# Kernel tuning notes

Hardware: AMD Instinct MI355X
Metric: run time of the kernel (lower is better)

Reference implementation:

```python
import jax, jax.numpy as jnp
import numpy as np

B, HIMG, WIMG = 256, 64, 64
U, K, HID, O, A, V = 8, 4, 128, 4, 7, 400
EMB = ((HIMG - 1) // 2 - 2) * ((WIMG - 1) // 2 - 2) * 64  # 53824
CV = EMB // U  # comm value size 6728
DK, DKC = 64, 32  # input / comm attention key sizes


def conv2d(x, w, b):
    y = jax.lax.conv_general_dilated(x, w, (1, 1), 'VALID',
                                     dimension_numbers=('NCHW', 'OIHW', 'NCHW'))
    return y + b[None, :, None, None]


def maxpool2(x):
    return jax.lax.reduce_window(x, -jnp.inf, jax.lax.max,
                                 (1, 1, 2, 2), (1, 1, 2, 2), 'VALID')


def setup_inputs() -> dict:
    key = jax.random.key(0)
    ks = jax.random.split(key, 26)
    n = lambda i, shape, sc: (jax.random.normal(ks[i], shape, jnp.float32) * sc)
    return {
        'x': jax.random.uniform(ks[0], (B, HIMG, WIMG, 3), jnp.float32),
        'hx': n(1, (B, U, HID), 0.1),
        'cx': n(2, (B, U, HID), 0.1),
        'option': jax.random.uniform(ks[3], (B, O), jnp.float32),
        'conv1_w': n(4, (16, 3, 2, 2), 0.2), 'conv1_b': jnp.zeros((16,), jnp.float32),
        'conv2_w': n(5, (32, 16, 2, 2), 0.1), 'conv2_b': jnp.zeros((32,), jnp.float32),
        'conv3_w': n(6, (64, 32, 2, 2), 0.08), 'conv3_b': jnp.zeros((64,), jnp.float32),
        'Wk': n(7, (EMB, DK), 0.01), 'bk': jnp.zeros((DK,), jnp.float32),
        'Wv': n(8, (EMB, V), 0.01), 'bv': jnp.zeros((V,), jnp.float32),
        'Wq': n(9, (O, U, HID, DK), 0.05),
        'Wi': n(10, (U, V, 4 * HID), 0.05),
        'Wh': n(11, (U, HID, 4 * HID), 0.05),
        'b_lstm': jnp.zeros((U, 4 * HID), jnp.float32),
        'Wqc': n(12, (U, HID, DKC), 0.05),
        'Wkc': n(13, (U, HID, DKC), 0.05),
        'Wvc': n(14, (U, HID, CV), 0.05),
        'Wout': n(15, (U, CV, HID), 0.01),
        'pi_w': n(16, (O, HID, A), 0.05),
        'pi_b': n(17, (O, A), 0.05),
    }


def reference(x, hx, cx, option, conv1_w, conv1_b, conv2_w, conv2_b, conv3_w,
              conv3_b, Wk, bk, Wv, bv, Wq, Wi, Wh, b_lstm, Wqc, Wkc, Wvc,
              Wout, pi_w, pi_b):
    # conv trunk: NHWC -> NCHW (as torch transposes), conv/relu/pool stack
    h = jnp.transpose(x, (0, 3, 1, 2))
    h = maxpool2(jax.nn.relu(conv2d(h, conv1_w, conv1_b)))
    h = jax.nn.relu(conv2d(h, conv2_w, conv2_b))
    h = jax.nn.relu(conv2d(h, conv3_w, conv3_b))
    emb = h.reshape(h.shape[0], -1)  # (B, EMB)

    # RIM input attention: real input + null row, per-unit option-conditioned queries
    xin = jnp.stack([emb, jnp.zeros_like(emb)], axis=1)     # (B, 2, EMB)
    k_in = xin @ Wk + bk                                     # (B, 2, DK)
    v_in = xin @ Wv + bv                                     # (B, 2, V)
    Wq_o = jnp.einsum('bo,ouhk->buhk', option, Wq)           # option-selected query weights
    q = jnp.einsum('buh,buhk->buk', hx, Wq_o)                # (B, U, DK)
    scores = jnp.einsum('buk,bnk->bun', q, k_in) / jnp.sqrt(jnp.float32(DK))
    probs = jax.nn.softmax(scores, axis=-1)                  # (B, U, 2)
    attn_in = jnp.einsum('bun,bnv->buv', probs, v_in)        # (B, U, V)

    # top-k active-unit mask (units attending most to the real input)
    real = probs[:, :, 0]
    _, idx = jax.lax.top_k(real, K)
    mask = jnp.zeros((real.shape[0], U), real.dtype)
    mask = mask.at[jnp.arange(real.shape[0])[:, None], idx].set(1.0)

    # per-unit LSTM (grouped weights)
    pre = (jnp.einsum('buv,uvg->bug', attn_in, Wi)
           + jnp.einsum('buh,uhg->bug', hx, Wh) + b_lstm)
    i_g, f_g, g_g, o_g = jnp.split(pre, 4, axis=-1)
    c_new = jax.nn.sigmoid(f_g) * cx + jax.nn.sigmoid(i_g) * jnp.tanh(g_g)
    h_new = jax.nn.sigmoid(o_g) * jnp.tanh(c_new)

    # communication attention among units; inactive queries masked out
    qc = jnp.einsum('buh,uhk->buk', h_new, Wqc)
    kc = jnp.einsum('buh,uhk->buk', h_new, Wkc)
    vc = jnp.einsum('buh,uhv->buv', h_new, Wvc)              # (B, U, CV)
    cs = jnp.einsum('buk,bnk->bun', qc, kc) / jnp.sqrt(jnp.float32(DKC))
    cp = jax.nn.softmax(cs, axis=-1) * mask[:, :, None]
    ctx = jnp.einsum('bun,bnv->buv', cp, vc)                 # (B, U, CV)
    h_comm = h_new + jnp.einsum('buv,uvh->buh', ctx, Wout)

    m = mask[:, :, None]
    hy = m * h_comm + (1.0 - m) * hx
    cy = m * c_new + (1.0 - m) * cx

    logits = jnp.einsum('buh,oha->boa', hy, pi_w) + pi_b     # (B, O, A)
    action_probs = jax.nn.softmax(logits, axis=-1)
    return action_probs, hy, cy
```

## Files before the change

### kernel.cpp

```cpp
#include <hip/hip_runtime.h>
#include <math.h>

namespace {
constexpr int NB  = 256;
constexpr int NU  = 8;
constexpr int NKT = 4;
constexpr int NH  = 128;
constexpr int NO  = 4;
constexpr int NA  = 7;
constexpr int NV  = 400;
constexpr int NE  = 53824;
constexpr int NCV = 6728;
constexpr int NDK = 64;
constexpr int NDKC= 32;

constexpr int H1 = 31, W1 = 31;
constexpr int H2 = 30, W2 = 30;
constexpr int H3 = 29, W3 = 29;
}

typedef __attribute__((ext_vector_type(8))) short bf16x8_t;
typedef __attribute__((ext_vector_type(4))) float f32x4_t;

__device__ __forceinline__ unsigned short f2bf(float f) {
    unsigned int u = __float_as_uint(f);
    u += 0x7FFFu + ((u >> 16) & 1u);
    return (unsigned short)(u >> 16);
}
__device__ __forceinline__ float bf2f(unsigned short h) {
    return __uint_as_float((unsigned int)h << 16);
}

__global__ __launch_bounds__(256)
void k_conv1(const float* __restrict__ x, const float* __restrict__ w,
             const float* __restrict__ bias, float* __restrict__ out)
{
    __shared__ float ws[16*3*2*2];
    __shared__ float bs[16];
    int tid = threadIdx.x;
    if (tid < 192) ws[tid] = w[tid];
    if (tid < 16)  bs[tid] = bias[tid];
    __syncthreads();
    long idx = (long)blockIdx.x*256 + tid;
    if (idx >= (long)NB*16*H1*W1) return;
    int pw = idx % W1; long t = idx / W1;
    int ph = t % H1; t /= H1;
    int oc = t % 16; int b = t / 16;
    float mx = 0.f;
#pragma unroll
    for (int dh = 0; dh < 2; ++dh)
#pragma unroll
    for (int dw = 0; dw < 2; ++dw) {
        int h = 2*ph + dh, ww = 2*pw + dw;
        float s = bs[oc];
#pragma unroll
        for (int kh = 0; kh < 2; ++kh)
#pragma unroll
        for (int kw = 0; kw < 2; ++kw) {
            const float* xp = x + (((long)b*64 + (h+kh))*64 + (ww+kw))*3;
#pragma unroll
            for (int ic = 0; ic < 3; ++ic)
                s += xp[ic] * ws[((oc*3+ic)*2+kh)*2+kw];
        }
        mx = fmaxf(mx, s);
    }
    out[idx] = mx;
}

template<int OC, int IC, int HIN, int WIN, int HOUT, int WOUT>
__global__ __launch_bounds__(256)
void conv2x2_gemm(const float* __restrict__ in, const float* __restrict__ w,
                  const float* __restrict__ bias, float* __restrict__ out)
{
    constexpr int K    = IC*4;
    constexpr int TY   = OC/4;
    constexpr int TX   = 256/TY;
    constexpr int NT   = TX*4;
    constexpr int SPAT = HOUT*WOUT;
    constexpr int NBLK = (SPAT + NT - 1)/NT;

    const int b  = blockIdx.x / NBLK;
    const int n0 = (blockIdx.x % NBLK) * NT;

    __shared__ __align__(16) float As[16][OC+4];
    __shared__ __align__(16) float Bs[16][NT];

    const int tid = threadIdx.x;
    const int tx = tid % TX, ty = tid / TX;
    float acc[4][4] = {};
    const float* inb = in + (long)b*IC*HIN*WIN;

    for (int kk = 0; kk < K; kk += 16) {
#pragma unroll
        for (int i = 0; i < OC*16/256; ++i) {
            int lin = tid + i*256;
            int m = lin / 16, k = lin % 16;
            As[k][m] = w[m*K + kk + k];
        }
#pragma unroll
        for (int i = 0; i < 16*NT/256; ++i) {
            int lin = tid + i*256;
            int k = lin / NT, n = lin % NT;
            int gk = kk + k;
            int ic = gk >> 2, tap = gk & 3;
            int s = n0 + n;
            float v = 0.f;
            if (s < SPAT) {
                int oh = s / WOUT, ow = s % WOUT;
                v = inb[(ic*HIN + oh + (tap>>1))*WIN + ow + (tap&1)];
            }
            Bs[k][n] = v;
        }
        __syncthreads();
#pragma unroll
        for (int k = 0; k < 16; ++k) {
            float4 a4 = *reinterpret_cast<const float4*>(&As[k][ty*4]);
            float4 b4 = *reinterpret_cast<const float4*>(&Bs[k][tx*4]);
            float av[4] = {a4.x,a4.y,a4.z,a4.w};
            float bw[4] = {b4.x,b4.y,b4.z,b4.w};
#pragma unroll
            for (int i = 0; i < 4; ++i)
#pragma unroll
            for (int j = 0; j < 4; ++j) acc[i][j] += av[i]*bw[j];
        }
        __syncthreads();
    }
#pragma unroll
    for (int i = 0; i < 4; ++i) {
        int gm = ty*4 + i;
        float bi = bias[gm];
#pragma unroll
        for (int j = 0; j < 4; ++j) {
            int s = n0 + tx*4 + j;
            if (s < SPAT)
                out[((long)b*OC + gm)*SPAT + s] = fmaxf(acc[i][j] + bi, 0.f);
        }
    }
}

__global__ __launch_bounds__(256)
void k_cvt(const float* __restrict__ in, unsigned short* __restrict__ out, long n)
{
    long i = ((long)blockIdx.x*256 + threadIdx.x) * 8;
    if (i >= n) return;
    float4 a = *(const float4*)(in + i);
    float4 b = *(const float4*)(in + i + 4);
    uint4 u;
    u.x = (unsigned)f2bf(a.x) | ((unsigned)f2bf(a.y) << 16);
    u.y = (unsigned)f2bf(a.z) | ((unsigned)f2bf(a.w) << 16);
    u.z = (unsigned)f2bf(b.x) | ((unsigned)f2bf(b.y) << 16);
    u.w = (unsigned)f2bf(b.z) | ((unsigned)f2bf(b.w) << 16);
    *(uint4*)(out + i) = u;
}

__global__ __launch_bounds__(256)
void k_f2bt(const float* __restrict__ in, unsigned short* __restrict__ out,
            int R, int Cc, long sIn)
{
    __shared__ unsigned short t[32][33];
    const int b = blockIdx.z;
    const int r0 = blockIdx.y * 32, c0 = blockIdx.x * 32;
    const float* ip = in + (long)b * sIn;
    unsigned short* op = out + (long)b * sIn;
    const int tid = threadIdx.x;
    {
        int rr = tid >> 3, c4 = (tid & 7) * 4;
        int gr = r0 + rr;
        unsigned short h0=0,h1=0,h2=0,h3=0;
        if (gr < R) {
            if (c0 + c4 + 3 < Cc) {
                float4 f = *(const float4*)(ip + (long)gr*Cc + c0 + c4);
                h0=f2bf(f.x); h1=f2bf(f.y); h2=f2bf(f.z); h3=f2bf(f.w);
            } else {
                if (c0+c4+0 < Cc) h0 = f2bf(ip[(long)gr*Cc + c0+c4+0]);
                if (c0+c4+1 < Cc) h1 = f2bf(ip[(long)gr*Cc + c0+c4+1]);
                if (c0+c4+2 < Cc) h2 = f2bf(ip[(long)gr*Cc + c0+c4+2]);
                if (c0+c4+3 < Cc) h3 = f2bf(ip[(long)gr*Cc + c0+c4+3]);
            }
        }
        t[rr][c4+0]=h0; t[rr][c4+1]=h1; t[rr][c4+2]=h2; t[rr][c4+3]=h3;
    }
    __syncthreads();
    {
        int cc = tid >> 3, r4 = (tid & 7) * 4;
        int gc = c0 + cc;
        if (gc < Cc && r0 + r4 < R) {
            if (r0 + r4 + 3 < R) {
                *(ushort4*)(op + (long)gc*R + r0 + r4) =
                    make_ushort4(t[r4+0][cc], t[r4+1][cc], t[r4+2][cc], t[r4+3][cc]);
            } else {
#pragma unroll
                for (int j = 0; j < 4; ++j)
                    if (r0 + r4 + j < R) op[(long)gc*R + r0 + r4 + j] = t[r4+j][cc];
            }
        }
    }
}

template<int ROWS, bool F32>
__device__ __forceinline__ void stage_tile(const void* __restrict__ Av, long lda,
                                           int m0, int kk, int kEnd, int Mlim,
                                           unsigned short* lds, int tid)
{
#pragma unroll
    for (int i = 0; i < ROWS/64; ++i) {
        int row = (tid >> 2) + i*64;
        int blk = tid & 3;
        long gm = m0 + row;
        long gk = kk + blk*8;
        ushort4 lo = make_ushort4(0,0,0,0), hi = make_ushort4(0,0,0,0);
        if (gm < Mlim && gk < kEnd) {
            if (F32) {
                const float* A = (const float*)Av + gm*lda + gk;
                float4 f0 = *(const float4*)(A);
                float4 f1 = *(const float4*)(A + 4);
                lo = make_ushort4(f2bf(f0.x),f2bf(f0.y),f2bf(f0.z),f2bf(f0.w));
                hi = make_ushort4(f2bf(f1.x),f2bf(f1.y),f2bf(f1.z),f2bf(f1.w));
            } else {
                const unsigned short* A = (const unsigned short*)Av + gm*lda + gk;
                lo = *(const ushort4*)(A);
                hi = *(const ushort4*)(A + 4);
            }
        }
        int p = (blk ^ (row & 3)) << 3;
        *(ushort4*)&lds[row*32 + p]     = lo;
        *(ushort4*)&lds[row*32 + p + 4] = hi;
    }
}

template<int BM, int BN, bool AF32>
__global__ __launch_bounds__(256)
void bgemm_splitk(const void* __restrict__ Av, long lda, long sA,
                  const unsigned short* __restrict__ BT, long ldbt, long sB,
                  float* __restrict__ Cpart,
                  int M, int N, int K, int nsplit, int kChunk)
{
    constexpr int MR = BM/32, NR = BN/32;
    const int z = blockIdx.z;
    const int batch = z / nsplit, split = z - batch*nsplit;
    const int kStart = split * kChunk;
    const int kEnd = (kStart + kChunk < K) ? (kStart + kChunk) : K;
    const int m0 = blockIdx.y * BM;
    const int n0 = blockIdx.x * BN;

    __shared__ __align__(16) unsigned short As[BM*32];
    __shared__ __align__(16) unsigned short Bs[BN*32];

    const int tid = threadIdx.x;
    const int wave = tid >> 6, lane = tid & 63;
    const int wr = wave >> 1, wc = wave & 1;
    const int lr = lane & 15, lk = lane >> 4;
    const int rbase = wr*(BM/2), cbase = wc*(BN/2);

    const void* Ab = AF32 ? (const void*)((const float*)Av + (long)batch*sA)
                          : (const void*)((const unsigned short*)Av + (long)batch*sA);
    const unsigned short* Bb = BT + (long)batch*sB;

    f32x4_t acc[MR][NR];
#pragma unroll
    for (int i = 0; i < MR; ++i)
#pragma unroll
    for (int j = 0; j < NR; ++j)
        acc[i][j] = (f32x4_t){0.f,0.f,0.f,0.f};

    for (int kk = kStart; kk < kEnd; kk += 32) {
        stage_tile<BM,AF32>(Ab, lda, m0, kk, kEnd, M, As, tid);
        stage_tile<BN,false>((const void*)Bb, ldbt, n0, kk, kEnd, N, Bs, tid);
        __syncthreads();
        bf16x8_t af[MR], bfv[NR];
#pragma unroll
        for (int i = 0; i < MR; ++i) {
            int row = rbase + i*16 + lr;
            af[i] = *(const bf16x8_t*)&As[row*32 + ((lk ^ (row & 3)) << 3)];
        }
#pragma unroll
        for (int j = 0; j < NR; ++j) {
            int col = cbase + j*16 + lr;
            bfv[j] = *(const bf16x8_t*)&Bs[col*32 + ((lk ^ (col & 3)) << 3)];
        }
#pragma unroll
        for (int i = 0; i < MR; ++i)
#pragma unroll
        for (int j = 0; j < NR; ++j)
            acc[i][j] = __builtin_amdgcn_mfma_f32_16x16x32_bf16(af[i], bfv[j], acc[i][j], 0, 0, 0);
        __syncthreads();
    }

    const long cb2 = (long)z * M * N;
#pragma unroll
    for (int i = 0; i < MR; ++i) {
#pragma unroll
        for (int r = 0; r < 4; ++r) {
            int gm = m0 + rbase + i*16 + lk*4 + r;
            if (gm >= M) continue;
#pragma unroll
            for (int j = 0; j < NR; ++j) {
                int gn = n0 + cbase + j*16 + lr;
                if (gn < N) Cpart[cb2 + (long)gm*N + gn] = acc[i][j][r];
            }
        }
    }
}

template<bool AF32>
__global__ __launch_bounds__(256)
void bgemm_direct(const void* __restrict__ Av, long lda, long sA,
                  const unsigned short* __restrict__ BT, long ldbt, long sB,
                  unsigned short* __restrict__ Cout, long ldc, long sC,
                  int M, int N, int K)
{
    const int batch = blockIdx.z;
    const int m0 = blockIdx.y * 128;
    const int n0 = blockIdx.x * 128;

    __shared__ __align__(16) unsigned short As[128*32];
    __shared__ __align__(16) unsigned short Bs[128*32];

    const int tid = threadIdx.x;
    const int wave = tid >> 6, lane = tid & 63;
    const int wr = wave >> 1, wc = wave & 1;
    const int lr = lane & 15, lk = lane >> 4;

    const void* Ab = AF32 ? (const void*)((const float*)Av + (long)batch*sA)
                          : (const void*)((const unsigned short*)Av + (long)batch*sA);
    const unsigned short* Bb = BT + (long)batch*sB;

    f32x4_t acc[4][4];
#pragma unroll
    for (int i = 0; i < 4; ++i)
#pragma unroll
    for (int j = 0; j < 4; ++j)
        acc[i][j] = (f32x4_t){0.f,0.f,0.f,0.f};

    for (int kk = 0; kk < K; kk += 32) {
        stage_tile<128,AF32>(Ab, lda, m0, kk, K, M, As, tid);
        stage_tile<128,false>((const void*)Bb, ldbt, n0, kk, K, N, Bs, tid);
        __syncthreads();
        bf16x8_t af[4], bfv[4];
#pragma unroll
        for (int i = 0; i < 4; ++i) {
            int row = wr*64 + i*16 + lr;
            af[i]  = *(const bf16x8_t*)&As[row*32 + ((lk ^ (row & 3)) << 3)];
            int col = wc*64 + i*16 + lr;
            bfv[i] = *(const bf16x8_t*)&Bs[col*32 + ((lk ^ (col & 3)) << 3)];
        }
#pragma unroll
        for (int i = 0; i < 4; ++i)
#pragma unroll
        for (int j = 0; j < 4; ++j)
            acc[i][j] = __builtin_amdgcn_mfma_f32_16x16x32_bf16(af[i], bfv[j], acc[i][j], 0, 0, 0);
        __syncthreads();
    }

    unsigned short* C = Cout + (long)batch * sC;
#pragma unroll
    for (int i = 0; i < 4; ++i) {
#pragma unroll
        for (int r = 0; r < 4; ++r) {
            int gm = m0 + wr*64 + i*16 + lk*4 + r;
            if (gm >= M) continue;
#pragma unroll
            for (int j = 0; j < 4; ++j) {
                int gn = n0 + wc*64 + j*16 + lr;
                if (gn < N) C[(long)gm*ldc + gn] = f2bf(acc[i][j][r]);
            }
        }
    }
}

template<bool AF32>
__global__ __launch_bounds__(256)
void bgemm_f32(const void* __restrict__ Av, long lda, long sA,
               const unsigned short* __restrict__ BT, long ldbt, long sB,
               float* __restrict__ Cout, long ldc, long sC,
               int M, int N, int K)
{
    const int batch = blockIdx.z;
    const int m0 = blockIdx.y * 64;
    const int n0 = blockIdx.x * 64;

    __shared__ __align__(16) unsigned short As[64*32];
    __shared__ __align__(16) unsigned short Bs[64*32];

    const int tid = threadIdx.x;
    const int wave = tid >> 6, lane = tid & 63;
    const int wr = wave >> 1, wc = wave & 1;
    const int lr = lane & 15, lk = lane >> 4;
    const int rbase = wr*32, cbase = wc*32;

    const void* Ab = AF32 ? (const void*)((const float*)Av + (long)batch*sA)
                          : (const void*)((const unsigned short*)Av + (long)batch*sA);
    const unsigned short* Bb = BT + (long)batch*sB;

    f32x4_t acc[2][2];
#pragma unroll
    for (int i = 0; i < 2; ++i)
#pragma unroll
    for (int j = 0; j < 2; ++j)
        acc[i][j] = (f32x4_t){0.f,0.f,0.f,0.f};

    for (int kk = 0; kk < K; kk += 32) {
        stage_tile<64,AF32>(Ab, lda, m0, kk, K, M, As, tid);
        stage_tile<64,false>((const void*)Bb, ldbt, n0, kk, K, N, Bs, tid);
        __syncthreads();
        bf16x8_t af[2], bfv[2];
#pragma unroll
        for (int i = 0; i < 2; ++i) {
            int row = rbase + i*16 + lr;
            af[i] = *(const bf16x8_t*)&As[row*32 + ((lk ^ (row & 3)) << 3)];
            int col = cbase + i*16 + lr;
            bfv[i] = *(const bf16x8_t*)&Bs[col*32 + ((lk ^ (col & 3)) << 3)];
        }
#pragma unroll
        for (int i = 0; i < 2; ++i)
#pragma unroll
        for (int j = 0; j < 2; ++j)
            acc[i][j] = __builtin_amdgcn_mfma_f32_16x16x32_bf16(af[i], bfv[j], acc[i][j], 0, 0, 0);
        __syncthreads();
    }

    float* C = Cout + (long)batch * sC;
#pragma unroll
    for (int i = 0; i < 2; ++i) {
#pragma unroll
        for (int r = 0; r < 4; ++r) {
            int gm = m0 + rbase + i*16 + lk*4 + r;
            if (gm >= M) continue;
#pragma unroll
            for (int j = 0; j < 2; ++j) {
                int gn = n0 + cbase + j*16 + lr;
                if (gn < N) C[(long)gm*ldc + gn] = acc[i][j][r];
            }
        }
    }
}

__global__ __launch_bounds__(256)
void k0_gemm(const float* __restrict__ A, const float* __restrict__ B,
             float* __restrict__ Cpart, int K, int kChunk)
{
    const int z = blockIdx.x;
    const int kStart = z * kChunk;
    const int kEnd = (kStart + kChunk < K) ? (kStart + kChunk) : K;
    __shared__ __align__(16) float As[16][260];
    __shared__ __align__(16) float Bs[16][64];
    const int tid = threadIdx.x;
    const int tx = tid & 15, ty = tid >> 4;
    float acc[16][4] = {};
    for (int kk = kStart; kk < kEnd; kk += 16) {
#pragma unroll
        for (int i = 0; i < 4; ++i) {
            int row = (tid >> 2) + i*64;
            int k4 = (tid & 3) * 4;
            long gk = kk + k4;
            float4 f = {0,0,0,0};
            if (gk + 3 < (long)kEnd) f = *(const float4*)(A + (long)row*K + gk);
            else {
                if (gk+0 < kEnd) f.x = A[(long)row*K+gk+0];
                if (gk+1 < kEnd) f.y = A[(long)row*K+gk+1];
                if (gk+2 < kEnd) f.z = A[(long)row*K+gk+2];
                if (gk+3 < kEnd) f.w = A[(long)row*K+gk+3];
            }
            As[k4+0][row]=f.x; As[k4+1][row]=f.y; As[k4+2][row]=f.z; As[k4+3][row]=f.w;
        }
        {
            int k = tid >> 4, n = (tid & 15) * 4;
            long gk = kk + k;
            float4 f = {0,0,0,0};
            if (gk < kEnd) f = *(const float4*)(B + gk*64 + n);
            *(float4*)&Bs[k][n] = f;
        }
        __syncthreads();
#pragma unroll
        for (int k = 0; k < 16; ++k) {
            float4 b4 = *reinterpret_cast<const float4*>(&Bs[k][tx*4]);
            float bw[4] = {b4.x,b4.y,b4.z,b4.w};
#pragma unroll
            for (int i4 = 0; i4 < 4; ++i4) {
                float4 a4 = *reinterpret_cast<const float4*>(&As[k][ty*16 + i4*4]);
                float av[4] = {a4.x,a4.y,a4.z,a4.w};
#pragma unroll
                for (int r = 0; r < 4; ++r)
#pragma unroll
                for (int j = 0; j < 4; ++j) acc[i4*4+r][j] += av[r]*bw[j];
            }
        }
        __syncthreads();
    }
    float* cp = Cpart + (long)z*256*64;
#pragma unroll
    for (int i = 0; i < 16; ++i) {
        int gm = ty*16 + i;
#pragma unroll
        for (int j = 0; j < 4; ++j)
            cp[(long)gm*64 + tx*4 + j] = acc[i][j];
    }
}

__global__ __launch_bounds__(256)
void k_reduce_splitk(const float* __restrict__ Cpart, float* __restrict__ out,
                     long ldcOut, long sOut,
                     const float* __restrict__ bias, long sBias,
                     int nbatch, int M, int N, int nsplit)
{
    long idx = (long)blockIdx.x*256 + threadIdx.x;
    long total = (long)nbatch*M*N;
    if (idx >= total) return;
    int n = idx % N; long t = idx / N;
    int m = t % M; int bi = t / M;
    const float* p = Cpart + ((long)bi*nsplit)*((long)M*N) + (long)m*N + n;
    float s = bias ? bias[(long)bi*sBias + n] : 0.f;
#pragma unroll 8
    for (int si = 0; si < nsplit; ++si) s += p[(long)si*M*N];
    out[(long)bi*sOut + (long)m*ldcOut + n] = s;
}

__global__ __launch_bounds__(256)
void k_q(const float* __restrict__ opt, const float* __restrict__ hx,
         const float* __restrict__ Wq, float* __restrict__ q)
{
    int idx = blockIdx.x*256 + threadIdx.x;
    if (idx >= NB*NU*NDK) return;
    int k = idx & 63; int t = idx >> 6;
    int u = t & 7; int b = t >> 3;
    const float* hxr = hx + (long)(b*NU+u)*NH;
    float acc = 0.f;
    for (int o = 0; o < NO; ++o) {
        const float* w = Wq + ((long)(o*NU+u)*NH)*NDK + k;
        float s = 0.f;
        for (int h = 0; h < NH; ++h) s += hxr[h] * w[(long)h*NDK];
        acc += opt[b*NO+o] * s;
    }
    q[idx] = acc;
}

__global__ __launch_bounds__(64)
void k_attn(const float* __restrict__ q, const float* __restrict__ k0,
            const float* __restrict__ bk, const float* __restrict__ v0,
            const float* __restrict__ bv, float* __restrict__ attn,
            float* __restrict__ real)
{
    int bu = blockIdx.x;
    int lane = threadIdx.x;
    int b = bu >> 3;
    float qv = q[(long)bu*NDK + lane];
    float s0 = qv * k0[(long)b*NDK + lane];
    float s1 = qv * bk[lane];
    for (int off = 32; off; off >>= 1) {
        s0 += __shfl_xor(s0, off);
        s1 += __shfl_xor(s1, off);
    }
    s0 *= 0.125f; s1 *= 0.125f;
    float mx = fmaxf(s0, s1);
    float e0 = expf(s0-mx), e1 = expf(s1-mx);
    float inv = 1.f/(e0+e1);
    float p0 = e0*inv, p1 = e1*inv;
    if (lane == 0) real[bu] = p0;
    for (int v = lane; v < NV; v += 64)
        attn[(long)bu*NV + v] = p0*v0[(long)b*NV + v] + p1*bv[v];
}

__global__ void k_topk(const float* __restrict__ real, float* __restrict__ mask)
{
    int b = blockIdx.x*blockDim.x + threadIdx.x;
    if (b >= NB) return;
    float v[NU]; bool sel[NU];
#pragma unroll
    for (int i = 0; i < NU; ++i) { v[i] = real[b*NU+i]; sel[i] = false; }
    for (int t = 0; t < NKT; ++t) {
        int best = 0; float bvv = -1e30f;
#pragma unroll
        for (int i = 0; i < NU; ++i)
            if (!sel[i] && v[i] > bvv) { bvv = v[i]; best = i; }
        sel[best] = true;
    }
#pragma unroll
    for (int i = 0; i < NU; ++i) mask[b*NU+i] = sel[i] ? 1.f : 0.f;
}

__global__ __launch_bounds__(256)
void k_gates(const float* __restrict__ pre_i, const float* __restrict__ pre_h,
             const float* __restrict__ blstm, const float* __restrict__ cx,
             float* __restrict__ cn, float* __restrict__ hn)
{
    int idx = blockIdx.x*256 + threadIdx.x;
    if (idx >= NB*NU*NH) return;
    int h = idx & 127; int bu = idx >> 7;
    int u = bu & 7;
    const float* pi = pre_i + (long)bu*512;
    const float* ph = pre_h + (long)bu*512;
    const float* bl = blstm + (long)u*512;
    float ig = pi[h]     + ph[h]     + bl[h];
    float fg = pi[128+h] + ph[128+h] + bl[128+h];
    float gg = pi[256+h] + ph[256+h] + bl[256+h];
    float og = pi[384+h] + ph[384+h] + bl[384+h];
    float si = 1.f/(1.f+expf(-ig));
    float sf = 1.f/(1.f+expf(-fg));
    float so = 1.f/(1.f+expf(-og));
    float c = sf*cx[idx] + si*tanhf(gg);
    cn[idx] = c;
    hn[idx] = so*tanhf(c);
}

__global__ __launch_bounds__(256)
void k_qckc(const float* __restrict__ hn, const float* __restrict__ Wqc,
            const float* __restrict__ Wkc, float* __restrict__ qc,
            float* __restrict__ kc)
{
    int idx = blockIdx.x*256 + threadIdx.x;
    if (idx >= NB*NU*64) return;
    int j = idx & 63; int t = idx >> 6;
    int u = t & 7; int b = t >> 3;
    int k = j & 31;
    const float* W = (j < 32 ? Wqc : Wkc) + ((long)u*NH)*NDKC + k;
    const float* h = hn + (long)(b*NU+u)*NH;
    float s = 0.f;
    for (int hh = 0; hh < NH; ++hh) s += h[hh]*W[(long)hh*NDKC];
    (j < 32 ? qc : kc)[(b*NU+u)*NDKC + k] = s;
}

__global__ __launch_bounds__(64)
void k_cp(const float* __restrict__ qc, const float* __restrict__ kc,
          const float* __restrict__ mask, float* __restrict__ cp)
{
    int b = blockIdx.x;
    int lane = threadIdx.x;
    int u = lane >> 3, n = lane & 7;
    const float* qr = qc + (long)(b*NU+u)*NDKC;
    const float* kr = kc + (long)(b*NU+n)*NDKC;
    float d = 0.f;
    for (int k = 0; k < NDKC; ++k) d += qr[k]*kr[k];
    d *= 0.17677669529663687f;
    float mx = d;
    for (int off = 4; off; off >>= 1) mx = fmaxf(mx, __shfl_xor(mx, off, 8));
    float e = expf(d-mx);
    float sm = e;
    for (int off = 4; off; off >>= 1) sm += __shfl_xor(sm, off, 8);
    cp[b*64 + lane] = (e/sm) * mask[b*NU+u];
}

__global__ __launch_bounds__(256)
void k_ctx(const unsigned short* __restrict__ vc, const float* __restrict__ cp,
           unsigned short* __restrict__ ctx)
{
    int b = blockIdx.y;
    int v = blockIdx.x*256 + threadIdx.x;
    __shared__ float cps[64];
    if (threadIdx.x < 64) cps[threadIdx.x] = cp[b*64 + threadIdx.x];
    __syncthreads();
    if (v >= NCV) return;
    float vv[NU];
#pragma unroll
    for (int n = 0; n < NU; ++n) vv[n] = bf2f(vc[((long)(b*NU+n))*NCV + v]);
#pragma unroll
    for (int u = 0; u < NU; ++u) {
        float s = 0.f;
#pragma unroll
        for (int n = 0; n < NU; ++n) s += cps[u*8+n]*vv[n];
        ctx[((long)(b*NU+u))*NCV + v] = f2bf(s);
    }
}

__global__ __launch_bounds__(128)
void k_tail(const float* __restrict__ hn, const float* __restrict__ cn,
            const float* __restrict__ hcw, const float* __restrict__ hx,
            const float* __restrict__ cx, const float* __restrict__ mask,
            const float* __restrict__ piw, const float* __restrict__ pib,
            float* __restrict__ hy, float* __restrict__ cy,
            float* __restrict__ out)
{
    const int b = blockIdx.x;
    const int h = threadIdx.x;
    __shared__ float hs[128];
    __shared__ float lg[28];
    float s = 0.f;
#pragma unroll
    for (int u = 0; u < NU; ++u) {
        int idx = (b*NU+u)*NH + h;
        float m = mask[b*NU+u];
        float hyv = m*(hn[idx]+hcw[idx]) + (1.f-m)*hx[idx];
        float cyv = m*cn[idx] + (1.f-m)*cx[idx];
        hy[idx] = hyv; cy[idx] = cyv;
        s += hyv;
    }
    hs[h] = s;
    __syncthreads();
    if (h < 28) {
        int o = h / 7, a = h - o*7;
        float acc = pib[o*NA+a];
        for (int k = 0; k < NH; ++k) acc += hs[k] * piw[((long)o*NH+k)*NA + a];
        lg[h] = acc;
    }
    __syncthreads();
    if (h < NO) {
        float mx = lg[h*NA];
#pragma unroll
        for (int a = 1; a < NA; ++a) mx = fmaxf(mx, lg[h*NA+a]);
        float e[NA]; float sm = 0.f;
#pragma unroll
        for (int a = 0; a < NA; ++a) { e[a] = expf(lg[h*NA+a]-mx); sm += e[a]; }
        float inv = 1.f/sm;
#pragma unroll
        for (int a = 0; a < NA; ++a) out[(long)b*NO*NA + h*NA + a] = e[a]*inv;
    }
}

extern "C" void kernel_launch(void* const* d_in, const int* in_sizes, int n_in,
                              void* d_out, int out_size, void* d_ws, size_t ws_size,
                              hipStream_t stream) {
    const float* x    = (const float*)d_in[0];
    const float* hx   = (const float*)d_in[1];
    const float* cx   = (const float*)d_in[2];
    const float* opt  = (const float*)d_in[3];
    const float* c1w  = (const float*)d_in[4];
    const float* c1b  = (const float*)d_in[5];
    const float* c2w  = (const float*)d_in[6];
    const float* c2b  = (const float*)d_in[7];
    const float* c3w  = (const float*)d_in[8];
    const float* c3b  = (const float*)d_in[9];
    const float* Wk   = (const float*)d_in[10];
    const float* bk   = (const float*)d_in[11];
    const float* Wv   = (const float*)d_in[12];
    const float* bv   = (const float*)d_in[13];
    const float* Wq   = (const float*)d_in[14];
    const float* Wi   = (const float*)d_in[15];
    const float* Wh   = (const float*)d_in[16];
    const float* blstm= (const float*)d_in[17];
    const float* Wqc  = (const float*)d_in[18];
    const float* Wkc  = (const float*)d_in[19];
    const float* Wvc  = (const float*)d_in[20];
    const float* Wout = (const float*)d_in[21];
    const float* piw  = (const float*)d_in[22];
    const float* pib  = (const float*)d_in[23];

    float* out = (float*)d_out;
    float* hy  = out + (long)NB*NO*NA;
    float* cy  = hy + (long)NB*NU*NH;

    float* ws = (float*)d_ws;
    long o = 0;
    float* b_k0  = ws + o; o += 16384;
    float* b_v0  = ws + o; o += 102400;
    float* b_q   = ws + o; o += 131072;
    float* b_at  = ws + o; o += 819200;
    float* b_re  = ws + o; o += 2048;
    float* b_mk  = ws + o; o += 2048;
    float* b_pre = ws + o; o += 1048576;
    float* b_cn  = ws + o; o += 262144;
    float* b_hn  = ws + o; o += 262144;
    float* b_qc  = ws + o; o += 65536;
    float* b_kc  = ws + o; o += 65536;
    float* b_cp  = ws + o; o += 16384;
    float* b_hc  = ws + o; o += 262144;
    float* b_hs  = ws + o; o += 32768;
    constexpr long P1OFF  = 3088384;
    constexpr long C2OFF  = 7024640;
    constexpr long EMBOFF = 14397440;
    constexpr long TOFF   = 28176384;
    constexpr long NEED   = TOFF + 5242880;
    if (ws_size < (size_t)NEED * sizeof(float)) return;

    float* p1    = ws + P1OFF;
    float* c2    = ws + C2OFF;
    float* emb   = ws + EMBOFF;
    float* partK = ws + TOFF;
    float* partV = ws + EMBOFF;
    unsigned short* emb16 = (unsigned short*)(ws + TOFF);
    unsigned short* WvT   = (unsigned short*)(ws + P1OFF);
    unsigned short* WiT   = (unsigned short*)(ws + TOFF);
    unsigned short* WhT   = (unsigned short*)(ws + TOFF + 819200);
    float* pre_h          = ws + TOFF + 819200 + 262144;
    unsigned short* WvcT  = (unsigned short*)(ws + P1OFF);
    unsigned short* WoutT = (unsigned short*)(ws + P1OFF + 3444736);
    float* partW          = ws + P1OFF + 2*3444736;
    unsigned short* vc16  = (unsigned short*)(ws + EMBOFF);
    unsigned short* ctx16 = (unsigned short*)(ws + EMBOFF + 6889472);

    k_conv1<<<(NB*16*H1*W1 + 255)/256, 256, 0, stream>>>(x, c1w, c1b, p1);
    conv2x2_gemm<32,16,H1,W1,H2,W2><<<NB*((H2*W2+127)/128), 256, 0, stream>>>(p1, c2w, c2b, c2);
    conv2x2_gemm<64,32,H2,W2,H3,W3><<<NB*((H3*W3+63)/64), 256, 0, stream>>>(c2, c3w, c3b, emb);

    k_f2bt<<<dim3(13, 1682, 1), 256, 0, stream>>>(Wv, WvT, NE, NV, 0);

    k0_gemm<<<320, 256, 0, stream>>>(emb, Wk, partK, NE, 176);
    k_reduce_splitk<<<(NB*NDK + 255)/256, 256, 0, stream>>>(
        partK, b_k0, NDK, 0, bk, 0, 1, NB, NDK, 320);

    k_cvt<<<((long)NB*NE/8 + 255)/256, 256, 0, stream>>>(emb, emb16, (long)NB*NE);

    bgemm_splitk<128,128,false><<<dim3(4,2,87), 256, 0, stream>>>(
        emb16, NE, 0, WvT, NE, 0, partV, NB, NV, NE, 87, 624);
    k_reduce_splitk<<<(NB*NV + 255)/256, 256, 0, stream>>>(
        partV, b_v0, NV, 0, bv, 0, 1, NB, NV, 87);

    k_q<<<(NB*NU*NDK + 255)/256, 256, 0, stream>>>(opt, hx, Wq, b_q);
    k_attn<<<NB*NU, 64, 0, stream>>>(b_q, b_k0, bk, b_v0, bv, b_at, b_re);
    k_topk<<<1, 256, 0, stream>>>(b_re, b_mk);

    k_f2bt<<<dim3(16, 13, 8), 256, 0, stream>>>(Wi, WiT, NV, 512, (long)NV*512);
    k_f2bt<<<dim3(16, 4, 8), 256, 0, stream>>>(Wh, WhT, NH, 512, (long)NH*512);
    bgemm_f32<true><<<dim3(8, 4, NU), 256, 0, stream>>>(
        b_at, (long)NU*NV, NV, WiT, NV, (long)512*NV,
        b_pre, (long)NU*512, 512, NB, 512, NV);
    bgemm_f32<true><<<dim3(8, 4, NU), 256, 0, stream>>>(
        hx, (long)NU*NH, NH, WhT, NH, (long)512*NH,
        pre_h, (long)NU*512, 512, NB, 512, NH);
    k_gates<<<(NB*NU*NH + 255)/256, 256, 0, stream>>>(b_pre, pre_h, blstm, cx, b_cn, b_hn);

    k_f2bt<<<dim3(211, 4, 8), 256, 0, stream>>>(Wvc, WvcT, NH, NCV, (long)NH*NCV);
    k_f2bt<<<dim3(4, 211, 8), 256, 0, stream>>>(Wout, WoutT, NCV, NH, (long)NCV*NH);

    bgemm_direct<true><<<dim3((NCV+127)/128, 2, NU), 256, 0, stream>>>(
        b_hn, (long)NU*NH, NH, WvcT, NH, (long)NCV*NH,
        vc16, (long)NU*NCV, NCV, NB, NCV, NH);

    k_qckc<<<(NB*NU*64 + 255)/256, 256, 0, stream>>>(b_hn, Wqc, Wkc, b_qc, b_kc);
    k_cp<<<NB, 64, 0, stream>>>(b_qc, b_kc, b_mk, b_cp);
    k_ctx<<<dim3((NCV+255)/256, NB), 256, 0, stream>>>(vc16, b_cp, ctx16);

    bgemm_splitk<64,64,false><<<dim3(2,4,NU*16), 256, 0, stream>>>(
        ctx16, (long)NU*NCV, NCV, WoutT, NCV, (long)NCV*NH,
        partW, NB, NH, NCV, 16, 448);
    k_reduce_splitk<<<(NU*NB*NH + 255)/256, 256, 0, stream>>>(
        partW, b_hc, (long)NU*NH, NH, nullptr, 0, NU, NB, NH, 16);

    k_tail<<<NB, 128, 0, stream>>>(b_hn, b_cn, b_hc, hx, cx, b_mk, piw, pib, hy, cy, out);
}
```

Baseline: 468.3 us.

## Fuse bf16 embedding conversion into conv3 epilogue and widen conv tiles

The conv GEMM kernel now emits a bf16 copy of its output directly, so the separate float-to-bf16 conversion pass over the full embedding is removed. Each thread also computes eight output columns instead of four, doubling the spatial tile and halving the conv block count, and the per-element spatial index math is hoisted out of the k loop. Because emb16 now overwrites the region that held partK, partK moves to the P1 region and the Wv transpose is reordered after the Wk GEMM. The wider tile raises register pressure, and the extra bf16 stores in the conv epilogue are scattered 2-byte writes.

New measurement: 485.9 us. +3.8%, slower.

```diff
diff --git a/kernel.cpp b/kernel.cpp
--- a/kernel.cpp
+++ b/kernel.cpp
@@ -70,14 +70,16 @@
 template<int OC, int IC, int HIN, int WIN, int HOUT, int WOUT>
 __global__ __launch_bounds__(256)
 void conv2x2_gemm(const float* __restrict__ in, const float* __restrict__ w,
-                  const float* __restrict__ bias, float* __restrict__ out)
+                  const float* __restrict__ bias, float* __restrict__ out,
+                  unsigned short* __restrict__ out16)
 {
     constexpr int K    = IC*4;
     constexpr int TY   = OC/4;
     constexpr int TX   = 256/TY;
-    constexpr int NT   = TX*4;
+    constexpr int NT   = TX*8;
     constexpr int SPAT = HOUT*WOUT;
     constexpr int NBLK = (SPAT + NT - 1)/NT;
+    constexpr int HNT  = NT/2;
 
     const int b  = blockIdx.x / NBLK;
     const int n0 = (blockIdx.x % NBLK) * NT;
@@ -87,8 +89,16 @@
 
     const int tid = threadIdx.x;
     const int tx = tid % TX, ty = tid / TX;
-    float acc[4][4] = {};
+    float acc[4][8] = {};
     const float* inb = in + (long)b*IC*HIN*WIN;
+
+    constexpr int COLS = NT/256 ? NT/256 : 1;
+    const int nIdx = (NT == 256) ? tid : (tid % NT);
+    int oh0 = 0, ow0 = 0; bool nOk = false;
+    {
+        int s = n0 + nIdx;
+        if (s < SPAT) { oh0 = s / WOUT; ow0 = s % WOUT; nOk = true; }
+    }
 
     for (int kk = 0; kk < K; kk += 16) {
 #pragma unroll
@@ -100,28 +110,26 @@
 #pragma unroll
         for (int i = 0; i < 16*NT/256; ++i) {
             int lin = tid + i*256;
-            int k = lin / NT, n = lin % NT;
+            int k = lin / NT;
             int gk = kk + k;
             int ic = gk >> 2, tap = gk & 3;
-            int s = n0 + n;
             float v = 0.f;
-            if (s < SPAT) {
-                int oh = s / WOUT, ow = s % WOUT;
-                v = inb[(ic*HIN + oh + (tap>>1))*WIN + ow + (tap&1)];
-            }
-            Bs[k][n] = v;
+            if (nOk)
+                v = inb[(ic*HIN + oh0 + (tap>>1))*WIN + ow0 + (tap&1)];
+            Bs[k][nIdx] = v;
         }
         __syncthreads();
 #pragma unroll
         for (int k = 0; k < 16; ++k) {
             float4 a4 = *reinterpret_cast<const float4*>(&As[k][ty*4]);
-            float4 b4 = *reinterpret_cast<const float4*>(&Bs[k][tx*4]);
+            float4 b4a = *reinterpret_cast<const float4*>(&Bs[k][tx*4]);
+            float4 b4b = *reinterpret_cast<const float4*>(&Bs[k][HNT + tx*4]);
             float av[4] = {a4.x,a4.y,a4.z,a4.w};
-            float bw[4] = {b4.x,b4.y,b4.z,b4.w};
+            float bw[8] = {b4a.x,b4a.y,b4a.z,b4a.w, b4b.x,b4b.y,b4b.z,b4b.w};
 #pragma unroll
             for (int i = 0; i < 4; ++i)
 #pragma unroll
-            for (int j = 0; j < 4; ++j) acc[i][j] += av[i]*bw[j];
+            for (int j = 0; j < 8; ++j) acc[i][j] += av[i]*bw[j];
         }
         __syncthreads();
     }
@@ -130,27 +138,15 @@
         int gm = ty*4 + i;
         float bi = bias[gm];
 #pragma unroll
-        for (int j = 0; j < 4; ++j) {
-            int s = n0 + tx*4 + j;
-            if (s < SPAT)
-                out[((long)b*OC + gm)*SPAT + s] = fmaxf(acc[i][j] + bi, 0.f);
-        }
-    }
-}
-
-__global__ __launch_bounds__(256)
-void k_cvt(const float* __restrict__ in, unsigned short* __restrict__ out, long n)
-{
-    long i = ((long)blockIdx.x*256 + threadIdx.x) * 8;
-    if (i >= n) return;
-    float4 a = *(const float4*)(in + i);
-    float4 b = *(const float4*)(in + i + 4);
-    uint4 u;
-    u.x = (unsigned)f2bf(a.x) | ((unsigned)f2bf(a.y) << 16);
-    u.y = (unsigned)f2bf(a.z) | ((unsigned)f2bf(a.w) << 16);
-    u.z = (unsigned)f2bf(b.x) | ((unsigned)f2bf(b.y) << 16);
-    u.w = (unsigned)f2bf(b.z) | ((unsigned)f2bf(b.w) << 16);
-    *(uint4*)(out + i) = u;
+        for (int j = 0; j < 8; ++j) {
+            int s = n0 + (j < 4 ? tx*4 + j : HNT + tx*4 + (j-4));
+            if (s < SPAT) {
+                float v = fmaxf(acc[i][j] + bi, 0.f);
+                out[((long)b*OC + gm)*SPAT + s] = v;
+                if (out16) out16[((long)b*OC + gm)*SPAT + s] = f2bf(v);
+            }
+        }
+    }
 }
 
 __global__ __launch_bounds__(256)
@@ -763,7 +759,7 @@
     float* p1    = ws + P1OFF;
     float* c2    = ws + C2OFF;
     float* emb   = ws + EMBOFF;
-    float* partK = ws + TOFF;
+    float* partK = ws + P1OFF;
     float* partV = ws + EMBOFF;
     unsigned short* emb16 = (unsigned short*)(ws + TOFF);
     unsigned short* WvT   = (unsigned short*)(ws + P1OFF);
@@ -777,16 +773,14 @@
     unsigned short* ctx16 = (unsigned short*)(ws + EMBOFF + 6889472);
 
     k_conv1<<<(NB*16*H1*W1 + 255)/256, 256, 0, stream>>>(x, c1w, c1b, p1);
-    conv2x2_gemm<32,16,H1,W1,H2,W2><<<NB*((H2*W2+127)/128), 256, 0, stream>>>(p1, c2w, c2b, c2);
-    conv2x2_gemm<64,32,H2,W2,H3,W3><<<NB*((H3*W3+63)/64), 256, 0, stream>>>(c2, c3w, c3b, emb);
-
-    k_f2bt<<<dim3(13, 1682, 1), 256, 0, stream>>>(Wv, WvT, NE, NV, 0);
+    conv2x2_gemm<32,16,H1,W1,H2,W2><<<NB*((H2*W2+255)/256), 256, 0, stream>>>(p1, c2w, c2b, c2, nullptr);
+    conv2x2_gemm<64,32,H2,W2,H3,W3><<<NB*((H3*W3+127)/128), 256, 0, stream>>>(c2, c3w, c3b, emb, emb16);
 
     k0_gemm<<<320, 256, 0, stream>>>(emb, Wk, partK, NE, 176);
     k_reduce_splitk<<<(NB*NDK + 255)/256, 256, 0, stream>>>(
         partK, b_k0, NDK, 0, bk, 0, 1, NB, NDK, 320);
 
-    k_cvt<<<((long)NB*NE/8 + 255)/256, 256, 0, stream>>>(emb, emb16, (long)NB*NE);
+    k_f2bt<<<dim3(13, 1682, 1), 256, 0, stream>>>(Wv, WvT, NE, NV, 0);
 
     bgemm_splitk<128,128,false><<<dim3(4,2,87), 256, 0, stream>>>(
         emb16, NE, 0, WvT, NE, 0, partV, NB, NV, NE, 87, 624);
```
